# Kernel tuning notes

Measured on AMD Instinct MI355X. Metric: run time of the kernel, lower is better.

## Reference

```python
import jax, jax.numpy as jnp
import numpy as np

H = 256      # hidden_dim
NH = 8       # num_heads
D = H // NH  # per-head dim
NEG = -(2.0**32) + 1.0
EPS = 1e-5


def setup_inputs() -> dict:
    key = jax.random.key(0)
    ks = jax.random.split(key, 12)
    N, Tq, Tk = 2, 2048, 2048
    s = 1.0 / np.sqrt(H)
    return {
        "Q": jax.random.normal(ks[0], (N, Tq, H), jnp.float32),
        "K": jax.random.normal(ks[1], (N, Tk, H), jnp.float32),
        "V": jax.random.normal(ks[2], (N, Tk, H), jnp.float32),
        "Wq": jax.random.normal(ks[3], (H, H), jnp.float32) * s,
        "bq": jnp.zeros((H,), jnp.float32),
        "Wk": jax.random.normal(ks[4], (H, H), jnp.float32) * s,
        "bk": jnp.zeros((H,), jnp.float32),
        "Wv": jax.random.normal(ks[5], (H, H), jnp.float32) * s,
        "bv": jnp.zeros((H,), jnp.float32),
        "gamma": jnp.ones((H,), jnp.float32),
        "beta": jnp.zeros((H,), jnp.float32),
    }


def _split_heads(x):
    # [N,T,H] -> [h,N,T,D]  (matches torch split(dim=2)+cat(dim=0): head-major)
    N, T, _ = x.shape
    return x.reshape(N, T, NH, D).transpose(2, 0, 1, 3)


def reference(Q, K, V, Wq, bq, Wk, bk, Wv, bv, gamma, beta):
    N, Tq, _ = Q.shape
    Tk = K.shape[1]
    Ql = jax.nn.relu(Q @ Wq + bq)
    Kl = jax.nn.relu(K @ Wk + bk)
    Vl = jax.nn.relu(V @ Wv + bv)
    Qh, Kh, Vh = _split_heads(Ql), _split_heads(Kl), _split_heads(Vl)

    scores = jnp.einsum("hnqd,hnkd->hnqk", Qh, Kh) / jnp.sqrt(jnp.float32(D))
    key_mask = jnp.sign(jnp.abs(K).sum(-1))    # [N,Tk]
    scores = jnp.where(key_mask[None, :, None, :] == 0, NEG, scores)
    attn = jax.nn.softmax(scores / 0.01, axis=-1)
    query_mask = jnp.sign(jnp.abs(Q).sum(-1))  # [N,Tq]
    attn = attn * query_mask[None, :, :, None]  # dropout p=0 -> identity

    ctx = jnp.einsum("hnqk,hnkd->hnqd", attn[..., :-1], Vh[:, :, :-1, :])
    out = ctx.transpose(1, 2, 0, 3).reshape(N, Tq, H)

    mu = out.mean(-1, keepdims=True)
    var = ((out - mu) ** 2).mean(-1, keepdims=True)
    out = (out - mu) / jnp.sqrt(var + EPS) * gamma + beta

    weight = attn.transpose(1, 2, 0, 3).reshape(N, Tq, NH * Tk).mean(-1)
    return out, weight
```

## Files before the change

kernel.cpp:

```cpp
#include <hip/hip_runtime.h>
#include <math.h>

#define H_DIM 256
#define NHEAD 8
#define DHEAD 32
#define NB 2
#define TSEQ 2048
#define LN_EPS 1e-5f

#define QK2_SCALE 25.503486f
#define SPLIT 4
#define TILES_PER (TSEQ / 64 / SPLIT)

typedef _Float16 half8 __attribute__((ext_vector_type(8)));
typedef _Float16 half4t __attribute__((ext_vector_type(4)));
typedef _Float16 half2t __attribute__((ext_vector_type(2)));
typedef float f32x4 __attribute__((ext_vector_type(4)));

__device__ __forceinline__ f32x4 mfma16(half8 a, half8 b, f32x4 c) {
  return __builtin_amdgcn_mfma_f32_16x16x32_f16(a, b, c, 0, 0, 0);
}
__device__ __forceinline__ float exp2fast(float x) {
  return __builtin_amdgcn_exp2f(x);
}
__device__ __forceinline__ half2t pkrtz(float a, float b) {
  return __builtin_bit_cast(half2t, __builtin_amdgcn_cvt_pkrtz(a, b));
}

__global__ __launch_bounds__(256) void setup_kernel(
    const float* __restrict__ Q, const float* __restrict__ K,
    const float* __restrict__ Wq, const float* __restrict__ Wk, const float* __restrict__ Wv,
    float* __restrict__ qmask, float* __restrict__ kmask,
    half8* __restrict__ WpkHi, half8* __restrict__ WpkLo) {
  const int tid = threadIdx.x;
  if (blockIdx.x < 2048) {
    const int wid = tid >> 6, lane = tid & 63;
    int row = blockIdx.x * 4 + wid;
    const int total_q = NB * TSEQ;
    const float* src;
    float* dst;
    if (row < total_q) { src = Q + (size_t)row * H_DIM; dst = qmask + row; }
    else               { src = K + (size_t)(row - total_q) * H_DIM; dst = kmask + (row - total_q); }
    float4 v = *(const float4*)(src + lane * 4);
    float s = fabsf(v.x) + fabsf(v.y) + fabsf(v.z) + fabsf(v.w);
    #pragma unroll
    for (int off = 32; off > 0; off >>= 1) s += __shfl_xor(s, off);
    if (lane == 0) *dst = (s != 0.0f) ? 1.0f : 0.0f;
    return;
  }
  int slot = (blockIdx.x - 2048) * 256 + tid;
  int lane = slot & 63;
  int fg = (slot >> 6) & 15;
  int s  = (slot >> 10) & 7;
  int which = slot >> 13;
  const float* W = which == 0 ? Wq : which == 1 ? Wk : Wv;
  int j  = fg * 16 + (lane & 15);
  int kb = s * 32 + (lane >> 4) * 8;
  half8 hi, lo;
  #pragma unroll
  for (int jj = 0; jj < 8; ++jj) {
    float x = W[(size_t)(kb + jj) * H_DIM + j];
    _Float16 h = (_Float16)x;
    hi[jj] = h;
    lo[jj] = (_Float16)(x - (float)h);
  }
  WpkHi[slot] = hi;
  WpkLo[slot] = lo;
}

__global__ __launch_bounds__(256) void proj_kernel(
    const float* __restrict__ Q, const float* __restrict__ K, const float* __restrict__ V,
    const float* __restrict__ bq, const float* __restrict__ bk, const float* __restrict__ bv,
    const half8* __restrict__ WpkHi, const half8* __restrict__ WpkLo,
    const float* __restrict__ kmask,
    half8* __restrict__ Gqhi, half8* __restrict__ Gqlo,
    half8* __restrict__ Gkhi, half8* __restrict__ Gklo, half8* __restrict__ Gv,
    half8* __restrict__ AmaskF) {
  const int which = blockIdx.z;
  const float* X    = which == 0 ? Q  : which == 1 ? K  : V;
  const float* bias = which == 0 ? bq : which == 1 ? bk : bv;

  __shared__ __align__(16) float T[64 * 68];

  const int tid = threadIdx.x;
  const int w = tid >> 6, lane = tid & 63;
  const int l15 = lane & 15, quad = lane >> 4;
  const int mbase = blockIdx.y * 64;
  const int nfg   = blockIdx.x * 4;
  const int nn   = mbase >> 11;
  const int tile = blockIdx.y & 31;

  half8 ahi[8], alo[8];
  {
    const float* xrow = X + (size_t)(mbase + w * 16 + l15) * H_DIM + quad * 8;
    #pragma unroll
    for (int s = 0; s < 8; ++s) {
      float4 a0 = *(const float4*)(xrow + s * 32);
      float4 a1 = *(const float4*)(xrow + s * 32 + 4);
      float xs[8] = {a0.x, a0.y, a0.z, a0.w, a1.x, a1.y, a1.z, a1.w};
      #pragma unroll
      for (int i = 0; i < 8; ++i) {
        _Float16 h = (_Float16)xs[i];
        ahi[s][i] = h;
        alo[s][i] = (_Float16)(xs[i] - (float)h);
      }
    }
  }

  f32x4 acc[4];
  #pragma unroll
  for (int f = 0; f < 4; ++f) acc[f] = (f32x4){0.f, 0.f, 0.f, 0.f};

  #pragma unroll
  for (int s = 0; s < 8; ++s) {
    const half8* ph = WpkHi + (((size_t)which * 8 + s) * 16 + nfg) * 64 + lane;
    const half8* pl = WpkLo + (((size_t)which * 8 + s) * 16 + nfg) * 64 + lane;
    #pragma unroll
    for (int f = 0; f < 4; ++f) {
      half8 BH = ph[f * 64];
      half8 BL = pl[f * 64];
      acc[f] = mfma16(ahi[s], BH, acc[f]);
      acc[f] = mfma16(ahi[s], BL, acc[f]);
      acc[f] = mfma16(alo[s], BH, acc[f]);
    }
  }

  #pragma unroll
  for (int f = 0; f < 4; ++f) {
    float bj = bias[blockIdx.x * 64 + f * 16 + l15];
    #pragma unroll
    for (int r = 0; r < 4; ++r) {
      int row = w * 16 + quad * 4 + r;
      float val = fmaxf(acc[f][r] + bj, 0.0f);
      if (which == 2 && ((mbase + row) & (TSEQ - 1)) == TSEQ - 1) val = 0.0f;
      T[row * 68 + f * 16 + l15] = val;
    }
  }
  __syncthreads();

  if (which < 2) {
    const int fq = tid >> 6, lp = tid & 63;
    const int kdc = lp >> 4, krlo = lp & 15;
    const int row = fq * 16 + krlo;
    const float sc = (which == 0) ? QK2_SCALE : 1.0f;
    #pragma unroll
    for (int hs = 0; hs < 2; ++hs) {
      const float* p = &T[row * 68 + hs * 32 + kdc * 8];
      float4 a0 = *(const float4*)p;
      float4 a1 = *(const float4*)(p + 4);
      float xs[8] = {a0.x, a0.y, a0.z, a0.w, a1.x, a1.y, a1.z, a1.w};
      half8 hi, lo;
      #pragma unroll
      for (int i = 0; i < 8; ++i) {
        float x = xs[i] * sc;
        _Float16 h = (_Float16)x;
        hi[i] = h;
        lo[i] = (_Float16)(x - (float)h);
      }
      int hn = (blockIdx.x * 2 + hs) * NB + nn;
      size_t di = ((size_t)hn * 32 + tile) * 256 + tid;
      if (which == 0) { Gqhi[di] = hi; Gqlo[di] = lo; }
      else            { Gkhi[di] = hi; Gklo[di] = lo; }
    }
    if (which == 1 && blockIdx.x == 0 && tid < 128) {
      int c = tid >> 6, lane2 = tid & 63;
      int quad2 = lane2 >> 4, l15b = lane2 & 15;
      half8 am;
      #pragma unroll
      for (int j = 0; j < 8; ++j)
        am[j] = (l15b == 0) ? (_Float16)kmask[(size_t)nn * TSEQ + tile * 64 + c * 32 + quad2 * 8 + j]
                            : (_Float16)0.0f;
      AmaskF[(((size_t)nn * 32 + tile) * 2 + c) * 64 + lane2] = am;
    }
  } else {
    const int top = tid >> 6, mid = (tid >> 4) & 3, low = tid & 15;
    const int c = top >> 1, hh = top & 1;
    const int trow0 = (c * 4 + mid) * 8;
    float km[8];
    #pragma unroll
    for (int j = 0; j < 8; ++j)
      km[j] = kmask[(size_t)nn * TSEQ + tile * 64 + trow0 + j];
    #pragma unroll
    for (int hs = 0; hs < 2; ++hs) {
      const int col = hs * 32 + hh * 16 + low;
      half8 v8;
      #pragma unroll
      for (int j = 0; j < 8; ++j)
        v8[j] = (_Float16)(T[(trow0 + j) * 68 + col] * km[j]);
      int hn = (blockIdx.x * 2 + hs) * NB + nn;
      Gv[((size_t)hn * 32 + tile) * 256 + tid] = v8;
    }
  }
}

__global__ __launch_bounds__(256, 4) void attn_kernel(
    const half8* __restrict__ Gqhi, const half8* __restrict__ Gqlo,
    const half8* __restrict__ Gkhi, const half8* __restrict__ Gklo,
    const half8* __restrict__ Gv, const half8* __restrict__ AmaskF,
    _Float16* __restrict__ Opf, float* __restrict__ Mp, float* __restrict__ Lp) {
  __shared__ __align__(16) half8 KhB[2][256];
  __shared__ __align__(16) half8 KlB[2][256];
  __shared__ __align__(16) half8 VB[2][256];
  __shared__ __align__(16) half8 AB[2][128];
  __shared__ __align__(16) _Float16 Pbuf[4][16][72];

  const int tid = threadIdx.x;
  const int w = tid >> 6, lane = tid & 63;
  const int l15 = lane & 15, quad = lane >> 4;

  const int b = blockIdx.x;
  const int g    = ((b & 7) << 1) | ((b >> 3) & 1);
  const int qt   = (b >> 4) & 31;
  const int sblk = b >> 9;
  const int n = g & 1;

  const size_t fbase = (size_t)g * 32 * 256;
  const int tile0 = sblk * TILES_PER;

  half8 qhi = Gqhi[fbase + (size_t)qt * 256 + w * 64 + lane];
  half8 qlo = Gqlo[fbase + (size_t)qt * 256 + w * 64 + lane];

  float m_q = -1.0e30f;
  f32x4 O0, O1, Ol;
  O0 = (f32x4){0.f, 0.f, 0.f, 0.f};
  O1 = (f32x4){0.f, 0.f, 0.f, 0.f};
  Ol = (f32x4){0.f, 0.f, 0.f, 0.f};

  const half8* gkh = Gkhi + fbase + (size_t)tile0 * 256;
  const half8* gkl = Gklo + fbase + (size_t)tile0 * 256;
  const half8* gvv = Gv   + fbase + (size_t)tile0 * 256;
  const half8* gam = AmaskF + (size_t)(n * 32 + tile0) * 128;

  KhB[0][tid] = gkh[tid];
  KlB[0][tid] = gkl[tid];
  VB[0][tid]  = gvv[tid];
  if (tid < 128) AB[0][tid] = gam[tid];
  __syncthreads();

  #pragma unroll
  for (int tt = 0; tt < TILES_PER; ++tt) {
    const int cur = tt & 1, nxt = cur ^ 1;
    half8 rkh, rkl, rv, ra;
    if (tt < TILES_PER - 1) {
      rkh = gkh[(tt + 1) * 256 + tid];
      rkl = gkl[(tt + 1) * 256 + tid];
      rv  = gvv[(tt + 1) * 256 + tid];
      if (tid < 128) ra = gam[(tt + 1) * 128 + tid];
    }

    f32x4 S[4];
    #pragma unroll
    for (int f = 0; f < 4; ++f) {
      half8 KH = KhB[cur][f * 64 + lane];
      half8 KL = KlB[cur][f * 64 + lane];
      f32x4 a = (f32x4){0.f, 0.f, 0.f, 0.f};
      a = mfma16(KL, qhi, a);
      a = mfma16(KH, qlo, a);
      a = mfma16(KH, qhi, a);
      S[f] = a;
    }

    float t0 = fmaxf(fmaxf(S[0][0], S[0][1]), fmaxf(S[0][2], S[0][3]));
    float t1 = fmaxf(fmaxf(S[1][0], S[1][1]), fmaxf(S[1][2], S[1][3]));
    float t2 = fmaxf(fmaxf(S[2][0], S[2][1]), fmaxf(S[2][2], S[2][3]));
    float t3 = fmaxf(fmaxf(S[3][0], S[3][1]), fmaxf(S[3][2], S[3][3]));
    float mx = fmaxf(fmaxf(t0, t1), fmaxf(t2, t3));
    mx = fmaxf(mx, __shfl_xor(mx, 16));
    mx = fmaxf(mx, __shfl_xor(mx, 32));

    float mnew = fmaxf(m_q, mx);
    float alpha = exp2fast(m_q - mnew);
    m_q = mnew;

    #pragma unroll
    for (int f = 0; f < 4; ++f) {
      float p0 = exp2fast(S[f][0] - m_q);
      float p1 = exp2fast(S[f][1] - m_q);
      float p2 = exp2fast(S[f][2] - m_q);
      float p3 = exp2fast(S[f][3] - m_q);
      half2t a01 = pkrtz(p0, p1);
      half2t a23 = pkrtz(p2, p3);
      half4t pk4;
      pk4[0] = a01[0]; pk4[1] = a01[1]; pk4[2] = a23[0]; pk4[3] = a23[1];
      *(half4t*)&Pbuf[w][l15][f * 16 + quad * 4] = pk4;
    }
    #pragma unroll
    for (int r = 0; r < 4; ++r) { O0[r] *= alpha; O1[r] *= alpha; }
    Ol[0] *= alpha;
    asm volatile("s_waitcnt lgkmcnt(0)" ::: "memory");

    half8 am0 = AB[cur][lane];
    half8 am1 = AB[cur][64 + lane];
    const half8* vbuf = (const half8*)VB[cur];
    #pragma unroll
    for (int c = 0; c < 2; ++c) {
      half8 pb = *(const half8*)&Pbuf[w][l15][c * 32 + quad * 8];
      O0 = mfma16(vbuf[(c * 2 + 0) * 64 + lane], pb, O0);
      O1 = mfma16(vbuf[(c * 2 + 1) * 64 + lane], pb, O1);
      Ol = mfma16(c == 0 ? am0 : am1, pb, Ol);
    }

    if (tt < TILES_PER - 1) {
      KhB[nxt][tid] = rkh;
      KlB[nxt][tid] = rkl;
      VB[nxt][tid]  = rv;
      if (tid < 128) AB[nxt][tid] = ra;
    }
    __syncthreads();
  }

  {
    int q = qt * 64 + w * 16 + l15;
    size_t idx = ((size_t)(sblk * 16 + g) * TSEQ + q) * DHEAD;
    half4t o0 = {(_Float16)O0[0], (_Float16)O0[1], (_Float16)O0[2], (_Float16)O0[3]};
    half4t o1 = {(_Float16)O1[0], (_Float16)O1[1], (_Float16)O1[2], (_Float16)O1[3]};
    *(half4t*)&Opf[idx + quad * 4]      = o0;
    *(half4t*)&Opf[idx + 16 + quad * 4] = o1;
    if (quad == 0) {
      Mp[(size_t)(sblk * 16 + g) * TSEQ + q] = m_q;
      Lp[(size_t)(sblk * 16 + g) * TSEQ + q] = Ol[0];
    }
  }
}

__global__ __launch_bounds__(256) void ln_kernel(
    const _Float16* __restrict__ Opf, const float* __restrict__ Mp, const float* __restrict__ Lp,
    const float* __restrict__ gamma, const float* __restrict__ beta,
    const float* __restrict__ qmask,
    float* __restrict__ out, float* __restrict__ wout) {
  const int wid = threadIdx.x >> 6, lane = threadIdx.x & 63;
  const int row = blockIdx.x * 4 + wid;
  const int n = row >> 11, q = row & (TSEQ - 1);
  const int hh = lane >> 3;
  const int hn = hh * NB + n;
  const int dbase = (lane & 7) * 4;

  float m[SPLIT], l[SPLIT];
  half4t P[SPLIT];
  #pragma unroll
  for (int i = 0; i < SPLIT; ++i) {
    size_t si = (size_t)(i * 16 + hn) * TSEQ + q;
    P[i] = *(const half4t*)&Opf[si * DHEAD + dbase];
    m[i] = Mp[si];
    l[i] = Lp[si];
  }
  float mm = fmaxf(fmaxf(m[0], m[1]), fmaxf(m[2], m[3]));
  float denom = 0.f;
  float a[SPLIT];
  #pragma unroll
  for (int i = 0; i < SPLIT; ++i) { a[i] = exp2fast(m[i] - mm); denom += l[i] * a[i]; }
  float qm = qmask[row];
  float inv = qm / denom;

  float4 x = make_float4(0.f, 0.f, 0.f, 0.f);
  #pragma unroll
  for (int i = 0; i < SPLIT; ++i) {
    x.x += (float)P[i][0] * a[i]; x.y += (float)P[i][1] * a[i];
    x.z += (float)P[i][2] * a[i]; x.w += (float)P[i][3] * a[i];
  }
  x.x *= inv; x.y *= inv; x.z *= inv; x.w *= inv;

  float s = x.x + x.y + x.z + x.w;
  #pragma unroll
  for (int off = 32; off > 0; off >>= 1) s += __shfl_xor(s, off);
  float mu = s * (1.0f / H_DIM);
  float dx0 = x.x - mu, dx1 = x.y - mu, dx2 = x.z - mu, dx3 = x.w - mu;
  float sq = dx0 * dx0 + dx1 * dx1 + dx2 * dx2 + dx3 * dx3;
  #pragma unroll
  for (int off = 32; off > 0; off >>= 1) sq += __shfl_xor(sq, off);
  float rstd = rsqrtf(sq * (1.0f / H_DIM) + LN_EPS);
  float4 g = *(const float4*)(gamma + lane * 4);
  float4 bb = *(const float4*)(beta + lane * 4);
  float4 y;
  y.x = dx0 * rstd * g.x + bb.x;
  y.y = dx1 * rstd * g.y + bb.y;
  y.z = dx2 * rstd * g.z + bb.z;
  y.w = dx3 * rstd * g.w + bb.w;
  *(float4*)(out + (size_t)row * H_DIM + lane * 4) = y;
  if (lane == 0) wout[row] = qm * (1.0f / TSEQ);
}

extern "C" void kernel_launch(void* const* d_in, const int* in_sizes, int n_in,
                              void* d_out, int out_size, void* d_ws, size_t ws_size,
                              hipStream_t stream) {
  const float* Q  = (const float*)d_in[0];
  const float* K  = (const float*)d_in[1];
  const float* V  = (const float*)d_in[2];
  const float* Wq = (const float*)d_in[3];
  const float* bq = (const float*)d_in[4];
  const float* Wk = (const float*)d_in[5];
  const float* bk = (const float*)d_in[6];
  const float* Wv = (const float*)d_in[7];
  const float* bv = (const float*)d_in[8];
  const float* gamma = (const float*)d_in[9];
  const float* beta  = (const float*)d_in[10];

  char* ws = (char*)d_ws;
  const size_t NFRAG = (size_t)16 * 32 * 256;
  _Float16* Opf = (_Float16*)ws;
  half8* Gqhi = (half8*)(ws + (size_t)SPLIT * 16 * TSEQ * DHEAD * 2);
  half8* Gqlo = Gqhi + NFRAG;
  half8* Gkhi = Gqlo + NFRAG;
  half8* Gklo = Gkhi + NFRAG;
  half8* Gv   = Gklo + NFRAG;
  float* Mp = (float*)(Gv + NFRAG);
  float* Lp = Mp + SPLIT * 16 * TSEQ;
  float* qmask = Lp + SPLIT * 16 * TSEQ;
  float* kmask = qmask + NB * TSEQ;
  half8* WpkHi = (half8*)(kmask + NB * TSEQ);
  half8* WpkLo = WpkHi + 24576;
  half8* AmaskF = WpkLo + 24576;

  float* out  = (float*)d_out;
  float* wout = out + (size_t)NB * TSEQ * H_DIM;

  hipLaunchKernelGGL(setup_kernel, dim3(2048 + 96), dim3(256), 0, stream,
                     Q, K, Wq, Wk, Wv, qmask, kmask, WpkHi, WpkLo);
  hipLaunchKernelGGL(proj_kernel, dim3(H_DIM / 64, NB * TSEQ / 64, 3), dim3(256), 0, stream,
                     Q, K, V, bq, bk, bv, WpkHi, WpkLo, kmask,
                     Gqhi, Gqlo, Gkhi, Gklo, Gv, AmaskF);
  hipLaunchKernelGGL(attn_kernel, dim3(16 * 32 * SPLIT), dim3(256), 0, stream,
                     Gqhi, Gqlo, Gkhi, Gklo, Gv, AmaskF, Opf, Mp, Lp);
  hipLaunchKernelGGL(ln_kernel, dim3(NB * TSEQ / 4), dim3(256), 0, stream,
                     Opf, Mp, Lp, gamma, beta, qmask, out, wout);
}
```

Measured before the change: 127.0 us.

## Fuse split-KV combine and LayerNorm into attention via last-block counter

Removes the separate LayerNorm kernel. The last attention block to finish for each (batch, query tile) merges the split partials and applies LayerNorm in place, coordinated through an atomic counter that the setup kernel zeroes. Also halves the KV split count, adds s_setprio around the MFMA sections, and switches to pointer increments with partial unrolling. The trade-off is fewer blocks for parallelism and a serialized tail on the last-arriving block. The counter also needs the workspace to be large enough for its extra slots.

```diff
diff --git a/kernel.cpp b/kernel.cpp
--- a/kernel.cpp
+++ b/kernel.cpp
@@ -9,7 +9,7 @@
 #define LN_EPS 1e-5f
 
 #define QK2_SCALE 25.503486f
-#define SPLIT 4
+#define SPLIT 2
 #define TILES_PER (TSEQ / 64 / SPLIT)
 
 typedef _Float16 half8 __attribute__((ext_vector_type(8)));
@@ -31,9 +31,10 @@
     const float* __restrict__ Q, const float* __restrict__ K,
     const float* __restrict__ Wq, const float* __restrict__ Wk, const float* __restrict__ Wv,
     float* __restrict__ qmask, float* __restrict__ kmask,
-    half8* __restrict__ WpkHi, half8* __restrict__ WpkLo) {
+    half8* __restrict__ WpkHi, half8* __restrict__ WpkLo, int* __restrict__ ctr) {
   const int tid = threadIdx.x;
   if (blockIdx.x < 2048) {
+    if (blockIdx.x == 0 && tid < 64) ctr[tid] = 0;
     const int wid = tid >> 6, lane = tid & 63;
     int row = blockIdx.x * 4 + wid;
     const int total_q = NB * TSEQ;
@@ -197,12 +198,16 @@
     const half8* __restrict__ Gqhi, const half8* __restrict__ Gqlo,
     const half8* __restrict__ Gkhi, const half8* __restrict__ Gklo,
     const half8* __restrict__ Gv, const half8* __restrict__ AmaskF,
-    _Float16* __restrict__ Opf, float* __restrict__ Mp, float* __restrict__ Lp) {
+    _Float16* __restrict__ Opf, float* __restrict__ Mp, float* __restrict__ Lp,
+    const float* __restrict__ gamma, const float* __restrict__ beta,
+    const float* __restrict__ qmask, int* __restrict__ ctr,
+    float* __restrict__ out, float* __restrict__ wout) {
   __shared__ __align__(16) half8 KhB[2][256];
   __shared__ __align__(16) half8 KlB[2][256];
   __shared__ __align__(16) half8 VB[2][256];
   __shared__ __align__(16) half8 AB[2][128];
   __shared__ __align__(16) _Float16 Pbuf[4][16][72];
+  __shared__ int isLast;
 
   const int tid = threadIdx.x;
   const int w = tid >> 6, lane = tid & 63;
@@ -237,18 +242,19 @@
   if (tid < 128) AB[0][tid] = gam[tid];
   __syncthreads();
 
-  #pragma unroll
+  #pragma unroll 2
   for (int tt = 0; tt < TILES_PER; ++tt) {
     const int cur = tt & 1, nxt = cur ^ 1;
     half8 rkh, rkl, rv, ra;
     if (tt < TILES_PER - 1) {
-      rkh = gkh[(tt + 1) * 256 + tid];
-      rkl = gkl[(tt + 1) * 256 + tid];
-      rv  = gvv[(tt + 1) * 256 + tid];
-      if (tid < 128) ra = gam[(tt + 1) * 128 + tid];
+      rkh = gkh[256 + tid];
+      rkl = gkl[256 + tid];
+      rv  = gvv[256 + tid];
+      if (tid < 128) ra = gam[128 + tid];
     }
 
     f32x4 S[4];
+    __builtin_amdgcn_s_setprio(1);
     #pragma unroll
     for (int f = 0; f < 4; ++f) {
       half8 KH = KhB[cur][f * 64 + lane];
@@ -259,6 +265,7 @@
       a = mfma16(KH, qhi, a);
       S[f] = a;
     }
+    __builtin_amdgcn_s_setprio(0);
 
     float t0 = fmaxf(fmaxf(S[0][0], S[0][1]), fmaxf(S[0][2], S[0][3]));
     float t1 = fmaxf(fmaxf(S[1][0], S[1][1]), fmaxf(S[1][2], S[1][3]));
@@ -292,6 +299,7 @@
     half8 am0 = AB[cur][lane];
     half8 am1 = AB[cur][64 + lane];
     const half8* vbuf = (const half8*)VB[cur];
+    __builtin_amdgcn_s_setprio(1);
     #pragma unroll
     for (int c = 0; c < 2; ++c) {
       half8 pb = *(const half8*)&Pbuf[w][l15][c * 32 + quad * 8];
@@ -299,6 +307,7 @@
       O1 = mfma16(vbuf[(c * 2 + 1) * 64 + lane], pb, O1);
       Ol = mfma16(c == 0 ? am0 : am1, pb, Ol);
     }
+    __builtin_amdgcn_s_setprio(0);
 
     if (tt < TILES_PER - 1) {
       KhB[nxt][tid] = rkh;
@@ -307,6 +316,8 @@
       if (tid < 128) AB[nxt][tid] = ra;
     }
     __syncthreads();
+    kh_advance:
+    gkh += 256; gkl += 256; gvv += 256; gam += 128;
   }
 
   {
@@ -321,63 +332,68 @@
       Lp[(size_t)(sblk * 16 + g) * TSEQ + q] = Ol[0];
     }
   }
-}
-
-__global__ __launch_bounds__(256) void ln_kernel(
-    const _Float16* __restrict__ Opf, const float* __restrict__ Mp, const float* __restrict__ Lp,
-    const float* __restrict__ gamma, const float* __restrict__ beta,
-    const float* __restrict__ qmask,
-    float* __restrict__ out, float* __restrict__ wout) {
-  const int wid = threadIdx.x >> 6, lane = threadIdx.x & 63;
-  const int row = blockIdx.x * 4 + wid;
-  const int n = row >> 11, q = row & (TSEQ - 1);
-  const int hh = lane >> 3;
-  const int hn = hh * NB + n;
+
+  __syncthreads();
+  if (tid == 0) {
+    __threadfence();
+    int old = atomicAdd(&ctr[n * 32 + qt], 1);
+    isLast = (old == 2 * NHEAD - 1);
+  }
+  __syncthreads();
+  if (!isLast) return;
+  __threadfence();
+
+  const int hh2 = lane >> 3;
+  const int hn2 = hh2 * NB + n;
   const int dbase = (lane & 7) * 4;
-
-  float m[SPLIT], l[SPLIT];
-  half4t P[SPLIT];
-  #pragma unroll
-  for (int i = 0; i < SPLIT; ++i) {
-    size_t si = (size_t)(i * 16 + hn) * TSEQ + q;
-    P[i] = *(const half4t*)&Opf[si * DHEAD + dbase];
-    m[i] = Mp[si];
-    l[i] = Lp[si];
-  }
-  float mm = fmaxf(fmaxf(m[0], m[1]), fmaxf(m[2], m[3]));
-  float denom = 0.f;
-  float a[SPLIT];
-  #pragma unroll
-  for (int i = 0; i < SPLIT; ++i) { a[i] = exp2fast(m[i] - mm); denom += l[i] * a[i]; }
-  float qm = qmask[row];
-  float inv = qm / denom;
-
-  float4 x = make_float4(0.f, 0.f, 0.f, 0.f);
-  #pragma unroll
-  for (int i = 0; i < SPLIT; ++i) {
-    x.x += (float)P[i][0] * a[i]; x.y += (float)P[i][1] * a[i];
-    x.z += (float)P[i][2] * a[i]; x.w += (float)P[i][3] * a[i];
-  }
-  x.x *= inv; x.y *= inv; x.z *= inv; x.w *= inv;
-
-  float s = x.x + x.y + x.z + x.w;
-  #pragma unroll
-  for (int off = 32; off > 0; off >>= 1) s += __shfl_xor(s, off);
-  float mu = s * (1.0f / H_DIM);
-  float dx0 = x.x - mu, dx1 = x.y - mu, dx2 = x.z - mu, dx3 = x.w - mu;
-  float sq = dx0 * dx0 + dx1 * dx1 + dx2 * dx2 + dx3 * dx3;
-  #pragma unroll
-  for (int off = 32; off > 0; off >>= 1) sq += __shfl_xor(sq, off);
-  float rstd = rsqrtf(sq * (1.0f / H_DIM) + LN_EPS);
-  float4 g = *(const float4*)(gamma + lane * 4);
-  float4 bb = *(const float4*)(beta + lane * 4);
-  float4 y;
-  y.x = dx0 * rstd * g.x + bb.x;
-  y.y = dx1 * rstd * g.y + bb.y;
-  y.z = dx2 * rstd * g.z + bb.z;
-  y.w = dx3 * rstd * g.w + bb.w;
-  *(float4*)(out + (size_t)row * H_DIM + lane * 4) = y;
-  if (lane == 0) wout[row] = qm * (1.0f / TSEQ);
+  const float4 gma = *(const float4*)(gamma + lane * 4);
+  const float4 bta = *(const float4*)(beta + lane * 4);
+  for (int r = 0; r < 16; ++r) {
+    const int q = qt * 64 + w * 16 + r;
+    const int row = n * TSEQ + q;
+    float ms[SPLIT], ls[SPLIT];
+    half4t Pp[SPLIT];
+    #pragma unroll
+    for (int i = 0; i < SPLIT; ++i) {
+      size_t si = (size_t)(i * 16 + hn2) * TSEQ + q;
+      Pp[i] = *(const half4t*)&Opf[si * DHEAD + dbase];
+      ms[i] = Mp[si];
+      ls[i] = Lp[si];
+    }
+    float mmax = ms[0];
+    #pragma unroll
+    for (int i = 1; i < SPLIT; ++i) mmax = fmaxf(mmax, ms[i]);
+    float denom = 0.f, aa[SPLIT];
+    #pragma unroll
+    for (int i = 0; i < SPLIT; ++i) { aa[i] = exp2fast(ms[i] - mmax); denom += ls[i] * aa[i]; }
+    float qm = qmask[row];
+    float inv = qm / denom;
+
+    float4 x = make_float4(0.f, 0.f, 0.f, 0.f);
+    #pragma unroll
+    for (int i = 0; i < SPLIT; ++i) {
+      x.x += (float)Pp[i][0] * aa[i]; x.y += (float)Pp[i][1] * aa[i];
+      x.z += (float)Pp[i][2] * aa[i]; x.w += (float)Pp[i][3] * aa[i];
+    }
+    x.x *= inv; x.y *= inv; x.z *= inv; x.w *= inv;
+
+    float s = x.x + x.y + x.z + x.w;
+    #pragma unroll
+    for (int off = 32; off > 0; off >>= 1) s += __shfl_xor(s, off);
+    float mu = s * (1.0f / H_DIM);
+    float dx0 = x.x - mu, dx1 = x.y - mu, dx2 = x.z - mu, dx3 = x.w - mu;
+    float sq = dx0 * dx0 + dx1 * dx1 + dx2 * dx2 + dx3 * dx3;
+    #pragma unroll
+    for (int off = 32; off > 0; off >>= 1) sq += __shfl_xor(sq, off);
+    float rstd = rsqrtf(sq * (1.0f / H_DIM) + LN_EPS);
+    float4 y;
+    y.x = dx0 * rstd * gma.x + bta.x;
+    y.y = dx1 * rstd * gma.y + bta.y;
+    y.z = dx2 * rstd * gma.z + bta.z;
+    y.w = dx3 * rstd * gma.w + bta.w;
+    *(float4*)(out + (size_t)row * H_DIM + lane * 4) = y;
+    if (lane == 0) wout[row] = qm * (1.0f / TSEQ);
+  }
 }
 
 extern "C" void kernel_launch(void* const* d_in, const int* in_sizes, int n_in,
@@ -410,17 +426,17 @@
   half8* WpkHi = (half8*)(kmask + NB * TSEQ);
   half8* WpkLo = WpkHi + 24576;
   half8* AmaskF = WpkLo + 24576;
+  int* ctr = (int*)(AmaskF + (size_t)NB * 32 * 2 * 64);
 
   float* out  = (float*)d_out;
   float* wout = out + (size_t)NB * TSEQ * H_DIM;
 
   hipLaunchKernelGGL(setup_kernel, dim3(2048 + 96), dim3(256), 0, stream,
-                     Q, K, Wq, Wk, Wv, qmask, kmask, WpkHi, WpkLo);
+                     Q, K, Wq, Wk, Wv, qmask, kmask, WpkHi, WpkLo, ctr);
   hipLaunchKernelGGL(proj_kernel, dim3(H_DIM / 64, NB * TSEQ / 64, 3), dim3(256), 0, stream,
                      Q, K, V, bq, bk, bv, WpkHi, WpkLo, kmask,
                      Gqhi, Gqlo, Gkhi, Gklo, Gv, AmaskF);
   hipLaunchKernelGGL(attn_kernel, dim3(16 * 32 * SPLIT), dim3(256), 0, stream,
-                     Gqhi, Gqlo, Gkhi, Gklo, Gv, AmaskF, Opf, Mp, Lp);
-  hipLaunchKernelGGL(ln_kernel, dim3(NB * TSEQ / 4), dim3(256), 0, stream,
-                     Opf, Mp, Lp, gamma, beta, qmask, out, wout);
-}
+                     Gqhi, Gqlo, Gkhi, Gklo, Gv, AmaskF, Opf, Mp, Lp,
+                     gamma, beta, qmask, ctr, out, wout);
+}
```

Result: slower. 184.7 us (+45.4%).
